# Kernel optimization log

Measured on AMD Instinct MI355X. Metric: run time of the kernel, lower is better.

## Reference

```python
import jax, jax.numpy as jnp
import numpy as np

NUM_NODES = 100_000
NUM_EDGES = 3_200_000
NUM_GRAPHS = 1_000


def setup_inputs() -> dict:
    key = jax.random.key(0)
    ks = jax.random.split(key, 10)
    x = jax.random.normal(ks[0], (NUM_NODES, 3), dtype=jnp.float32)
    edge_index = jax.random.randint(ks[1], (2, NUM_EDGES), 0, NUM_NODES, dtype=jnp.int64)
    edge_attr = jax.random.normal(ks[2], (NUM_EDGES, 1), dtype=jnp.float32)
    batch = jnp.sort(jax.random.randint(ks[3], (NUM_NODES,), 0, NUM_GRAPHS, dtype=jnp.int64))
    # parameters (Glorot-ish scale)
    W1 = jax.random.normal(ks[4], (3, 16), dtype=jnp.float32) * (1.0 / np.sqrt(3))
    b1 = jnp.zeros((16,), dtype=jnp.float32)
    W2 = jax.random.normal(ks[5], (16, 16), dtype=jnp.float32) * (1.0 / np.sqrt(16))
    b2 = jnp.zeros((16,), dtype=jnp.float32)
    Wl = jax.random.normal(ks[6], (16, 7), dtype=jnp.float32) * (1.0 / np.sqrt(16))
    bl = jnp.zeros((7,), dtype=jnp.float32)
    return {"x": x, "edge_index": edge_index, "edge_attr": edge_attr, "batch": batch,
            "W1": W1, "b1": b1, "W2": W2, "b2": b2, "Wl": Wl, "bl": bl}


def _gcn_conv(h, W, b, row, col, norm, num_nodes):
    # PyG GCNConv: h' = scatter_add(norm * (hW)[row] -> col) + b
    m = (h @ W)[row] * norm[:, None]                      # [E+N, d_out]
    out = jax.ops.segment_sum(m, col, num_segments=num_nodes)
    return out + b


def reference(x, edge_index, edge_attr, batch, W1, b1, W2, b2, Wl, bl):
    num_nodes = x.shape[0]
    # add self loops (GCNConv default), edge weight 1
    loops = jnp.arange(num_nodes, dtype=edge_index.dtype)
    row = jnp.concatenate([edge_index[0], loops])
    col = jnp.concatenate([edge_index[1], loops])
    # symmetric normalization: deg over target (col)
    deg = jax.ops.segment_sum(jnp.ones_like(col, dtype=x.dtype), col, num_segments=num_nodes)
    dis = jnp.where(deg > 0, jax.lax.rsqrt(deg), 0.0)
    norm = dis[row] * dis[col]                            # [E+N]

    h = _gcn_conv(x, W1, b1, row, col, norm, num_nodes)
    h = jax.nn.relu(h)
    h = _gcn_conv(h, W2, b2, row, col, norm, num_nodes)
    # global_add_pool
    g = jax.ops.segment_sum(h, batch, num_segments=NUM_GRAPHS)  # [G, 16]
    logits = g @ Wl + bl                                  # [G, 7]
    return jax.nn.log_softmax(logits, axis=1)
```

## Files before the change

### kernel.cpp

```cpp
#include <hip/hip_runtime.h>
#include <math.h>

#define CHUNK 8192
#define BSH 8
#define BNODES 256
#define RAWCAP 9216
#define MAXCELL 512


union H2 { unsigned int u; _Float16 h[2]; };

__global__ void k_init(int* tot, float* g, int nb, int G16) {
    int i = blockIdx.x * blockDim.x + threadIdx.x;
    if (i < nb)  tot[i] = 0;
    if (i < G16) g[i]   = 0.0f;
}

__global__ __launch_bounds__(512) void k_bin(
                      const int* __restrict__ row, const int* __restrict__ col,
                      int* __restrict__ temp, unsigned short* __restrict__ off,
                      int* __restrict__ tot, int E, int NBLK, int nb) {
    __shared__ int cnt[512];
    __shared__ int cur[512];
    __shared__ int sc[512];
    __shared__ int stage[CHUNK];
    int blk = blockIdx.x;
    int start = blk * CHUNK;
    int cs = E - start; if (cs > CHUNK) cs = CHUNK;
    int t = threadIdx.x;
    cnt[t] = 0;
    __syncthreads();
    for (int i = t; i < cs; i += 512) atomicAdd(&cnt[col[start + i] >> BSH], 1);
    __syncthreads();
    int c = cnt[t];
    sc[t] = c;
    __syncthreads();
    for (int o = 1; o < 512; o <<= 1) {
        int x = (t >= o) ? sc[t - o] : 0;
        __syncthreads();
        sc[t] += x;
        __syncthreads();
    }
    int excl = sc[t] - c;
    if (t < nb) {
        off[t * NBLK + blk] = (unsigned short)excl;
        if (c) atomicAdd(&tot[t], c);
    }
    if (t == 0) off[nb * NBLK + blk] = (unsigned short)cs;
    cur[t] = excl;
    __syncthreads();
    for (int i = t; i < cs; i += 512) {
        int cc = col[start + i];
        int rr = row[start + i];
        int p = atomicAdd(&cur[cc >> BSH], 1);
        stage[p] = (rr << BSH) | (cc & (BNODES - 1));
    }
    __syncthreads();
    for (int i = t; i < cs; i += 512) temp[start + i] = stage[i];
}

__global__ void k_base(const int* __restrict__ tot, int* __restrict__ base,
                       int* __restrict__ ptrS, int E, int nb, int N) {
    __shared__ int s[512];
    __shared__ int carry;
    int t = threadIdx.x;
    if (t == 0) carry = 0;
    __syncthreads();
    for (int b0 = 0; b0 < nb; b0 += 512) {
        int i = b0 + t;
        int v = (i < nb) ? tot[i] : 0;
        s[t] = v;
        __syncthreads();
        for (int o = 1; o < 512; o <<= 1) {
            int x = (t >= o) ? s[t - o] : 0;
            __syncthreads();
            s[t] += x;
            __syncthreads();
        }
        if (i < nb) base[i] = s[t] - v + carry;
        __syncthreads();
        if (t == 0) carry += s[511];
        __syncthreads();
    }
    if (t == 0) { base[nb] = E; ptrS[N] = E; }
}

__global__ __launch_bounds__(1024) void k_build(
                        const int* __restrict__ temp, const unsigned short* __restrict__ off,
                        const int* __restrict__ base, int* __restrict__ ptrS,
                        float* __restrict__ dinv, int* __restrict__ csr,
                        int NBLK, int N) {
    __shared__ int cnt[BNODES];
    __shared__ int cur[BNODES];
    __shared__ int cellstart[MAXCELL];
    __shared__ int soff[MAXCELL];
    __shared__ int wsum[16];
    __shared__ int raw[RAWCAP];
    __shared__ int stage[RAWCAP];
    int b = blockIdx.x;
    int t = threadIdx.x;
    int wid = t >> 6, lane = t & 63;
    if (t < BNODES) cnt[t] = 0;
    int len0 = 0;
    if (t < MAXCELL) {
        int s0v = 0;
        if (t < NBLK) {
            s0v = (int)off[b * NBLK + t];
            len0 = (int)off[(b + 1) * NBLK + t] - s0v;
        }
        soff[t] = s0v;
        int v = len0;
        for (int o = 1; o < 64; o <<= 1) {
            int u = __shfl_up(v, o, 64);
            if (lane >= o) v += u;
        }
        if (lane == 63) wsum[wid] = v;
        cellstart[t] = v - len0;
    }
    __syncthreads();
    if (t < MAXCELL) {
        int wb = 0;
        for (int i = 0; i < wid; ++i) wb += wsum[i];
        cellstart[t] += wb;
    }
    __syncthreads();
    int bb = base[b];
    int total = base[b + 1] - bb;
    int grp = t >> 4, gl = t & 15;
    for (int cell = grp; cell < NBLK; cell += 64) {
        int s0 = soff[cell];
        int rb = cellstart[cell];
        int len = ((cell + 1 < NBLK) ? cellstart[cell + 1] : total) - rb;
        const int* src = temp + cell * CHUNK + s0;
        for (int j = gl; j < len; j += 16) {
            int e = src[j];
            atomicAdd(&cnt[e & (BNODES - 1)], 1);
            int idx = rb + j;
            if (idx < RAWCAP) raw[idx] = e;
        }
    }
    __syncthreads();
    int c = 0, sincl = 0;
    if (t < BNODES) {
        c = cnt[t];
        sincl = c;
        for (int o = 1; o < 64; o <<= 1) {
            int u = __shfl_up(sincl, o, 64);
            if (lane >= o) sincl += u;
        }
        if (lane == 63) wsum[wid] = sincl;
    }
    __syncthreads();
    if (t < BNODES) {
        int wb2 = 0;
        for (int i = 0; i < wid; ++i) wb2 += wsum[i];
        int lstart = sincl - c + wb2;
        int node = (b << BSH) + t;
        if (node < N) {
            ptrS[node] = bb + lstart;
            dinv[node] = rsqrtf(1.0f + (float)c);
        }
        cur[t] = lstart;
    }
    __syncthreads();
    int cap = total > RAWCAP ? RAWCAP : total;
    for (int i = t; i < cap; i += 1024) {
        int e = raw[i];
        int p = atomicAdd(&cur[e & (BNODES - 1)], 1);
        int r = e >> BSH;
        if (p < RAWCAP) stage[p] = r;
        else            csr[bb + p] = r;
    }
    if (total > RAWCAP) {
        for (int cell = grp; cell < NBLK; cell += 64) {
            int s0 = soff[cell];
            int rb = cellstart[cell];
            int len = ((cell + 1 < NBLK) ? cellstart[cell + 1] : total) - rb;
            const int* src = temp + cell * CHUNK + s0;
            for (int j = gl; j < len; j += 16) {
                if (rb + j >= RAWCAP) {
                    int e = src[j];
                    int p = atomicAdd(&cur[e & (BNODES - 1)], 1);
                    int r = e >> BSH;
                    if (p < RAWCAP) stage[p] = r;
                    else            csr[bb + p] = r;
                }
            }
        }
    }
    __syncthreads();
    for (int i = t; i < cap; i += 1024) csr[bb + i] = stage[i];
}

__global__ void k_xw1(const float* __restrict__ x, const float* __restrict__ W1,
                      const float* __restrict__ dinv, unsigned int* __restrict__ h0u, int N) {
    int t = blockIdx.x * blockDim.x + threadIdx.x;
    if (t >= N * 8) return;
    int v = t >> 3, k = (t & 7) * 2;
    float x0 = x[v * 3 + 0], x1 = x[v * 3 + 1], x2 = x[v * 3 + 2];
    float d = dinv[v];
    H2 p;
    p.h[0] = (_Float16)(d * (x0 * W1[k] + x1 * W1[16 + k] + x2 * W1[32 + k]));
    p.h[1] = (_Float16)(d * (x0 * W1[k + 1] + x1 * W1[16 + k + 1] + x2 * W1[32 + k + 1]));
    h0u[t] = p.u;
}

__global__ void k_gather1(const int* __restrict__ ptrS, const int* __restrict__ csr,
                          const float* __restrict__ dinv, const unsigned int* __restrict__ h0u,
                          const float* __restrict__ W2, const float* __restrict__ b1,
                          unsigned int* __restrict__ h1u, int N) {
    __shared__ float sW[256];
    sW[threadIdx.x] = W2[threadIdx.x];
    __syncthreads();
    int t = blockIdx.x * blockDim.x + threadIdx.x;
    int v = t >> 3, gl = t & 7, k = gl * 2;
    if (v >= N) return;
    int s = ptrS[v], e = ptrS[v + 1];
    float al0 = 0.0f, ah0 = 0.0f, al1 = 0.0f, ah1 = 0.0f;
    int i = s;
    for (; i + 7 < e; i += 8) {
        int myr = __builtin_nontemporal_load(csr + i + gl);
#pragma unroll
        for (int q = 0; q < 8; ++q) {
            int r = __shfl(myr, q, 8);
            H2 p; p.u = h0u[r * 8 + gl];
            if (q & 1) { al1 += (float)p.h[0]; ah1 += (float)p.h[1]; }
            else       { al0 += (float)p.h[0]; ah0 += (float)p.h[1]; }
        }
    }
    if (i < e) {
        int rem = e - i;
        int myr = (gl < rem) ? __builtin_nontemporal_load(csr + i + gl) : 0;
        for (int q = 0; q < rem; ++q) {
            int r = __shfl(myr, q, 8);
            H2 p; p.u = h0u[r * 8 + gl];
            al0 += (float)p.h[0]; ah0 += (float)p.h[1];
        }
    }
    H2 selfp; selfp.u = h0u[v * 8 + gl];
    float d = dinv[v];
    float h_lo = fmaxf(d * (al0 + al1 + (float)selfp.h[0]) + b1[k], 0.0f);
    float h_hi = fmaxf(d * (ah0 + ah1 + (float)selfp.h[1]) + b1[k + 1], 0.0f);
    float o0 = 0.0f, o1 = 0.0f;
#pragma unroll
    for (int j = 0; j < 8; ++j) {
        float hl = __shfl(h_lo, j, 8);
        float hh = __shfl(h_hi, j, 8);
        o0 += hl * sW[(2 * j) * 16 + k]     + hh * sW[(2 * j + 1) * 16 + k];
        o1 += hl * sW[(2 * j) * 16 + k + 1] + hh * sW[(2 * j + 1) * 16 + k + 1];
    }
    H2 outp;
    outp.h[0] = (_Float16)(d * o0);
    outp.h[1] = (_Float16)(d * o1);
    __builtin_nontemporal_store(outp.u, h1u + v * 8 + gl);
}

__global__ void k_gather2(const int* __restrict__ ptrS, const int* __restrict__ csr,
                          const float* __restrict__ dinv, const unsigned int* __restrict__ h1u,
                          const float* __restrict__ b2, const int* __restrict__ batch,
                          float* __restrict__ g, int N) {
    int t = blockIdx.x * blockDim.x + threadIdx.x;
    int v = t >> 3, gl = t & 7, k = gl * 2;
    bool valid = (v < N);
    float val0 = 0.0f, val1 = 0.0f;
    int bg = 0;
    if (valid) {
        int s = ptrS[v], e = ptrS[v + 1];
        float al0 = 0.0f, ah0 = 0.0f, al1 = 0.0f, ah1 = 0.0f;
        int i = s;
        for (; i + 7 < e; i += 8) {
            int myr = __builtin_nontemporal_load(csr + i + gl);
#pragma unroll
            for (int q = 0; q < 8; ++q) {
                int r = __shfl(myr, q, 8);
                H2 p; p.u = h1u[r * 8 + gl];
                if (q & 1) { al1 += (float)p.h[0]; ah1 += (float)p.h[1]; }
                else       { al0 += (float)p.h[0]; ah0 += (float)p.h[1]; }
            }
        }
        if (i < e) {
            int rem = e - i;
            int myr = (gl < rem) ? __builtin_nontemporal_load(csr + i + gl) : 0;
            for (int q = 0; q < rem; ++q) {
                int r = __shfl(myr, q, 8);
                H2 p; p.u = h1u[r * 8 + gl];
                al0 += (float)p.h[0]; ah0 += (float)p.h[1];
            }
        }
        H2 selfp; selfp.u = h1u[v * 8 + gl];
        float d = dinv[v];
        val0 = d * (al0 + al1 + (float)selfp.h[0]) + b2[k];
        val1 = d * (ah0 + ah1 + (float)selfp.h[1]) + b2[k + 1];
        bg = batch[v];
    }
    int lane = threadIdx.x & 63;
    int bg0 = __shfl(bg, lane & 7, 64);
    bool uni = __all(valid && (bg == bg0));
    if (uni) {
        val0 += __shfl_xor(val0, 8, 64);
        val0 += __shfl_xor(val0, 16, 64);
        val0 += __shfl_xor(val0, 32, 64);
        val1 += __shfl_xor(val1, 8, 64);
        val1 += __shfl_xor(val1, 16, 64);
        val1 += __shfl_xor(val1, 32, 64);
        if (lane < 8) {
            atomicAdd(&g[bg * 16 + k], val0);
            atomicAdd(&g[bg * 16 + k + 1], val1);
        }
    } else if (valid) {
        atomicAdd(&g[bg * 16 + k], val0);
        atomicAdd(&g[bg * 16 + k + 1], val1);
    }
}

__global__ void k_head(const float* __restrict__ g, const float* __restrict__ Wl,
                       const float* __restrict__ bl, float* __restrict__ out, int G) {
    int gi = blockIdx.x * blockDim.x + threadIdx.x;
    if (gi >= G) return;
    float gv[16];
#pragma unroll
    for (int k = 0; k < 16; ++k) gv[k] = g[gi * 16 + k];
    float lo[7];
    float mx = -1e30f;
#pragma unroll
    for (int j = 0; j < 7; ++j) {
        float a = bl[j];
#pragma unroll
        for (int k = 0; k < 16; ++k) a += gv[k] * Wl[k * 7 + j];
        lo[j] = a;
        mx = fmaxf(mx, a);
    }
    float s = 0.0f;
#pragma unroll
    for (int j = 0; j < 7; ++j) s += expf(lo[j] - mx);
    float lse = mx + logf(s);
#pragma unroll
    for (int j = 0; j < 7; ++j) out[gi * 7 + j] = lo[j] - lse;
}

extern "C" void kernel_launch(void* const* d_in, const int* in_sizes, int n_in,
                              void* d_out, int out_size, void* d_ws, size_t ws_size,
                              hipStream_t stream) {
    const float* x    = (const float*)d_in[0];
    const int*   ei   = (const int*)d_in[1];
    const int*   batch = (const int*)d_in[3];
    const float* W1 = (const float*)d_in[4];
    const float* b1 = (const float*)d_in[5];
    const float* W2 = (const float*)d_in[6];
    const float* b2 = (const float*)d_in[7];
    const float* Wl = (const float*)d_in[8];
    const float* bl = (const float*)d_in[9];
    float* out = (float*)d_out;

    const int N = in_sizes[0] / 3;
    const int E = in_sizes[1] / 2;
    const int G = out_size / 7;

    const int* row = ei;
    const int* col = ei + E;

    const int NBLK = (E + CHUNK - 1) / CHUNK;
    const int nb   = (N + BNODES - 1) >> BSH;

    int* w = (int*)d_ws;
    float* dinv = (float*)w;            w += N;
    int*   ptrS = w;                    w += N + 1;
    int*   tot  = w;                    w += nb;
    int*   base = w;                    w += nb + 1;
    unsigned short* off = (unsigned short*)w;
    w += ((nb + 1) * NBLK + 1) / 2;
    int*   csr  = w;                    w += E;
    int tempsz = E > 32 * N ? E : 32 * N;
    int*   temp = w;                    w += tempsz;
    unsigned int* h0u = (unsigned int*)temp;
    unsigned int* h1u = (unsigned int*)(temp + 8 * N);
    float* g    = (float*)w;            w += 16 * G;

    const int TB = 256;
    const int n8  = N * 8;
    const int G16 = G * 16;
    const int initn = (G16 > nb) ? G16 : nb;

    k_init<<<(initn + TB - 1) / TB, TB, 0, stream>>>(tot, g, nb, G16);
    k_bin<<<NBLK, 512, 0, stream>>>(row, col, temp, off, tot, E, NBLK, nb);
    k_base<<<1, 512, 0, stream>>>(tot, base, ptrS, E, nb, N);
    k_build<<<nb, 1024, 0, stream>>>(temp, off, base, ptrS, dinv, csr, NBLK, N);
    k_xw1<<<(n8 + TB - 1) / TB, TB, 0, stream>>>(x, W1, dinv, h0u, N);
    k_gather1<<<(n8 + TB - 1) / TB, TB, 0, stream>>>(ptrS, csr, dinv, h0u, W2, b1, h1u, N);
    k_gather2<<<(n8 + TB - 1) / TB, TB, 0, stream>>>(ptrS, csr, dinv, h1u, b2, batch, g, N);
    k_head<<<(G + TB - 1) / TB, TB, 0, stream>>>(g, Wl, bl, out, G);
}
```

Baseline: 210.4 us.

## Fuse init and xW1 into other kernels, use wave-shuffle scans in binning

Removes the init kernel and the xW1 kernel. Bucket totals are now recomputed in k_base from the per-chunk offset table instead of being gathered with global atomics. The g buffer is zeroed inside k_base, and x·W1 scaled by dinv is computed at the end of k_build using shared dinv values. k_bin moves to 1024 threads and replaces its barrier-heavy Hillis-Steele scan with wave-level shuffle scans. The aim is to cut launch overhead and synchronisation. The cost is a serial column-sum over NBLK entries per thread in the single-block k_base, and h0u/h1u can no longer alias temp, so the workspace grows.

Measured after the change: 264.3 us. +25.6%, slower.

```diff
diff --git a/kernel.cpp b/kernel.cpp
--- a/kernel.cpp
+++ b/kernel.cpp
@@ -10,91 +10,95 @@
 
 union H2 { unsigned int u; _Float16 h[2]; };
 
-__global__ void k_init(int* tot, float* g, int nb, int G16) {
-    int i = blockIdx.x * blockDim.x + threadIdx.x;
-    if (i < nb)  tot[i] = 0;
-    if (i < G16) g[i]   = 0.0f;
-}
-
-__global__ __launch_bounds__(512) void k_bin(
+__global__ __launch_bounds__(1024) void k_bin(
                       const int* __restrict__ row, const int* __restrict__ col,
                       int* __restrict__ temp, unsigned short* __restrict__ off,
-                      int* __restrict__ tot, int E, int NBLK, int nb) {
+                      int E, int NBLK, int nb) {
     __shared__ int cnt[512];
     __shared__ int cur[512];
-    __shared__ int sc[512];
+    __shared__ int wsum[8];
     __shared__ int stage[CHUNK];
     int blk = blockIdx.x;
     int start = blk * CHUNK;
     int cs = E - start; if (cs > CHUNK) cs = CHUNK;
     int t = threadIdx.x;
-    cnt[t] = 0;
-    __syncthreads();
-    for (int i = t; i < cs; i += 512) atomicAdd(&cnt[col[start + i] >> BSH], 1);
-    __syncthreads();
-    int c = cnt[t];
-    sc[t] = c;
-    __syncthreads();
-    for (int o = 1; o < 512; o <<= 1) {
-        int x = (t >= o) ? sc[t - o] : 0;
-        __syncthreads();
-        sc[t] += x;
-        __syncthreads();
-    }
-    int excl = sc[t] - c;
-    if (t < nb) {
-        off[t * NBLK + blk] = (unsigned short)excl;
-        if (c) atomicAdd(&tot[t], c);
-    }
-    if (t == 0) off[nb * NBLK + blk] = (unsigned short)cs;
-    cur[t] = excl;
-    __syncthreads();
-    for (int i = t; i < cs; i += 512) {
+    int wid = t >> 6, lane = t & 63;
+    if (t < 512) cnt[t] = 0;
+    __syncthreads();
+    for (int i = t; i < cs; i += 1024) atomicAdd(&cnt[col[start + i] >> BSH], 1);
+    __syncthreads();
+    if (t < 512) {
+        int c = cnt[t];
+        int incl = c;
+        for (int o = 1; o < 64; o <<= 1) {
+            int u = __shfl_up(incl, o, 64);
+            if (lane >= o) incl += u;
+        }
+        if (lane == 63) wsum[wid] = incl;
+        cnt[t] = incl - c;
+    }
+    __syncthreads();
+    if (t < 512) {
+        int wb = 0;
+        for (int i = 0; i < wid; ++i) wb += wsum[i];
+        int excl = cnt[t] + wb;
+        if (t < nb) off[t * NBLK + blk] = (unsigned short)excl;
+        if (t == 0) off[nb * NBLK + blk] = (unsigned short)cs;
+        cur[t] = excl;
+    }
+    __syncthreads();
+    for (int i = t; i < cs; i += 1024) {
         int cc = col[start + i];
         int rr = row[start + i];
         int p = atomicAdd(&cur[cc >> BSH], 1);
         stage[p] = (rr << BSH) | (cc & (BNODES - 1));
     }
     __syncthreads();
-    for (int i = t; i < cs; i += 512) temp[start + i] = stage[i];
-}
-
-__global__ void k_base(const int* __restrict__ tot, int* __restrict__ base,
-                       int* __restrict__ ptrS, int E, int nb, int N) {
-    __shared__ int s[512];
-    __shared__ int carry;
+    for (int i = t; i < cs; i += 1024) temp[start + i] = stage[i];
+}
+
+__global__ __launch_bounds__(512) void k_base(
+                       const unsigned short* __restrict__ off, int* __restrict__ base,
+                       int* __restrict__ ptrS, float* __restrict__ g,
+                       int E, int nb, int NBLK, int N, int G16) {
+    __shared__ int rs[512];
+    __shared__ int wsum[8];
     int t = threadIdx.x;
-    if (t == 0) carry = 0;
-    __syncthreads();
-    for (int b0 = 0; b0 < nb; b0 += 512) {
-        int i = b0 + t;
-        int v = (i < nb) ? tot[i] : 0;
-        s[t] = v;
-        __syncthreads();
-        for (int o = 1; o < 512; o <<= 1) {
-            int x = (t >= o) ? s[t - o] : 0;
-            __syncthreads();
-            s[t] += x;
-            __syncthreads();
-        }
-        if (i < nb) base[i] = s[t] - v + carry;
-        __syncthreads();
-        if (t == 0) carry += s[511];
-        __syncthreads();
-    }
+    int wid = t >> 6, lane = t & 63;
+    int rsv = 0;
+    if (t <= nb) {
+        const unsigned short* orow = off + (size_t)t * NBLK;
+        for (int ch = 0; ch < NBLK; ++ch) rsv += orow[ch];
+    }
+    rs[t] = rsv;
+    __syncthreads();
+    int tb = (t < nb) ? rs[t + 1] - rs[t] : 0;
+    int incl = tb;
+    for (int o = 1; o < 64; o <<= 1) {
+        int u = __shfl_up(incl, o, 64);
+        if (lane >= o) incl += u;
+    }
+    if (lane == 63) wsum[wid] = incl;
+    __syncthreads();
+    int wb = 0;
+    for (int i = 0; i < wid; ++i) wb += wsum[i];
+    if (t < nb) base[t] = incl - tb + wb;
     if (t == 0) { base[nb] = E; ptrS[N] = E; }
+    for (int i = t; i < G16; i += 512) g[i] = 0.0f;
 }
 
 __global__ __launch_bounds__(1024) void k_build(
                         const int* __restrict__ temp, const unsigned short* __restrict__ off,
                         const int* __restrict__ base, int* __restrict__ ptrS,
                         float* __restrict__ dinv, int* __restrict__ csr,
-                        int NBLK, int N) {
+                        const float* __restrict__ x, const float* __restrict__ W1,
+                        unsigned int* __restrict__ h0u, int NBLK, int N) {
     __shared__ int cnt[BNODES];
     __shared__ int cur[BNODES];
     __shared__ int cellstart[MAXCELL];
     __shared__ int soff[MAXCELL];
     __shared__ int wsum[16];
+    __shared__ float sdinv[BNODES];
     __shared__ int raw[RAWCAP];
     __shared__ int stage[RAWCAP];
     int b = blockIdx.x;
@@ -156,9 +160,11 @@
         for (int i = 0; i < wid; ++i) wb2 += wsum[i];
         int lstart = sincl - c + wb2;
         int node = (b << BSH) + t;
+        float dv = rsqrtf(1.0f + (float)c);
+        sdinv[t] = dv;
         if (node < N) {
             ptrS[node] = bb + lstart;
-            dinv[node] = rsqrtf(1.0f + (float)c);
+            dinv[node] = dv;
         }
         cur[t] = lstart;
     }
@@ -190,19 +196,18 @@
     }
     __syncthreads();
     for (int i = t; i < cap; i += 1024) csr[bb + i] = stage[i];
-}
-
-__global__ void k_xw1(const float* __restrict__ x, const float* __restrict__ W1,
-                      const float* __restrict__ dinv, unsigned int* __restrict__ h0u, int N) {
-    int t = blockIdx.x * blockDim.x + threadIdx.x;
-    if (t >= N * 8) return;
-    int v = t >> 3, k = (t & 7) * 2;
-    float x0 = x[v * 3 + 0], x1 = x[v * 3 + 1], x2 = x[v * 3 + 2];
-    float d = dinv[v];
-    H2 p;
-    p.h[0] = (_Float16)(d * (x0 * W1[k] + x1 * W1[16 + k] + x2 * W1[32 + k]));
-    p.h[1] = (_Float16)(d * (x0 * W1[k + 1] + x1 * W1[16 + k + 1] + x2 * W1[32 + k + 1]));
-    h0u[t] = p.u;
+    for (int i = t; i < BNODES * 8; i += 1024) {
+        int vl = i >> 3, k2 = i & 7, k = k2 * 2;
+        int v = (b << BSH) + vl;
+        if (v < N) {
+            float x0 = x[v * 3 + 0], x1 = x[v * 3 + 1], x2 = x[v * 3 + 2];
+            float d = sdinv[vl];
+            H2 p;
+            p.h[0] = (_Float16)(d * (x0 * W1[k]     + x1 * W1[16 + k]     + x2 * W1[32 + k]));
+            p.h[1] = (_Float16)(d * (x0 * W1[k + 1] + x1 * W1[16 + k + 1] + x2 * W1[32 + k + 1]));
+            h0u[v * 8 + k2] = p.u;
+        }
+    }
 }
 
 __global__ void k_gather1(const int* __restrict__ ptrS, const int* __restrict__ csr,
@@ -365,27 +370,22 @@
     int* w = (int*)d_ws;
     float* dinv = (float*)w;            w += N;
     int*   ptrS = w;                    w += N + 1;
-    int*   tot  = w;                    w += nb;
     int*   base = w;                    w += nb + 1;
     unsigned short* off = (unsigned short*)w;
     w += ((nb + 1) * NBLK + 1) / 2;
     int*   csr  = w;                    w += E;
-    int tempsz = E > 32 * N ? E : 32 * N;
-    int*   temp = w;                    w += tempsz;
-    unsigned int* h0u = (unsigned int*)temp;
-    unsigned int* h1u = (unsigned int*)(temp + 8 * N);
+    int*   temp = w;                    w += E;
+    unsigned int* h0u = (unsigned int*)w;  w += 8 * N;
+    unsigned int* h1u = (unsigned int*)w;  w += 8 * N;
     float* g    = (float*)w;            w += 16 * G;
 
     const int TB = 256;
     const int n8  = N * 8;
     const int G16 = G * 16;
-    const int initn = (G16 > nb) ? G16 : nb;
-
-    k_init<<<(initn + TB - 1) / TB, TB, 0, stream>>>(tot, g, nb, G16);
-    k_bin<<<NBLK, 512, 0, stream>>>(row, col, temp, off, tot, E, NBLK, nb);
-    k_base<<<1, 512, 0, stream>>>(tot, base, ptrS, E, nb, N);
-    k_build<<<nb, 1024, 0, stream>>>(temp, off, base, ptrS, dinv, csr, NBLK, N);
-    k_xw1<<<(n8 + TB - 1) / TB, TB, 0, stream>>>(x, W1, dinv, h0u, N);
+
+    k_bin<<<NBLK, 1024, 0, stream>>>(row, col, temp, off, E, NBLK, nb);
+    k_base<<<1, 512, 0, stream>>>(off, base, ptrS, g, E, nb, NBLK, N, G16);
+    k_build<<<nb, 1024, 0, stream>>>(temp, off, base, ptrS, dinv, csr, x, W1, h0u, NBLK, N);
     k_gather1<<<(n8 + TB - 1) / TB, TB, 0, stream>>>(ptrS, csr, dinv, h0u, W2, b1, h1u, N);
     k_gather2<<<(n8 + TB - 1) / TB, TB, 0, stream>>>(ptrS, csr, dinv, h1u, b2, batch, g, N);
     k_head<<<(G + TB - 1) / TB, TB, 0, stream>>>(g, Wl, bl, out, G);
```
